# Performance work log

Measured on AMD Instinct MI355X. Metric: run time of the kernel, lower is better.

The kernel has to match this reference:

```python
import jax, jax.numpy as jnp
import numpy as np

BITS = 4
DIM = 64
N_LEVELS = 2 ** BITS


def _build_lloyd_max_codebook(bits=BITS, dim=DIM, n_samples=200000, n_iter=200, seed=0):
    """Lloyd-Max scalar quantizer for one coordinate of a random unit vector in R^dim."""
    rng = np.random.default_rng(seed)
    raw = rng.standard_normal((n_samples, dim)).astype(np.float32)
    unit = raw / np.linalg.norm(raw, axis=-1, keepdims=True)
    samples = unit[:, 0].astype(np.float64)
    n_levels = 2 ** bits
    sorted_samples = np.sort(samples)
    q_pos = np.linspace(0.5 / n_levels, 1.0 - 0.5 / n_levels, n_levels)
    idx_init = np.clip((q_pos * n_samples).astype(np.int64), 0, n_samples - 1)
    codebook = sorted_samples[idx_init].copy()
    for _ in range(n_iter):
        assignments = np.argmin(np.abs(samples[:, None] - codebook[None, :]), axis=1)
        counts = np.bincount(assignments, minlength=n_levels)
        sums = np.bincount(assignments, weights=samples, minlength=n_levels)
        new_cb = np.where(counts > 0, sums / np.maximum(counts, 1), codebook)
        delta = np.max(np.abs(new_cb - codebook))
        codebook = new_cb
        if delta < 1e-9:
            break
    return np.sort(codebook).astype(np.float32)


def _rotation_matrix(dim=DIM, seed=42):
    rng = np.random.default_rng(seed)
    g = rng.standard_normal((dim, dim)).astype(np.float32)
    q, _ = np.linalg.qr(g)
    return q.astype(np.float32)


def setup_inputs() -> dict:
    key = jax.random.key(0)
    x = jax.random.normal(key, (2, 32, 4096, DIM), dtype=jnp.float32)  # [B, H, S, dim]
    codebook = jnp.asarray(_build_lloyd_max_codebook())  # [16]
    R = jnp.asarray(_rotation_matrix())                  # [dim, dim]
    return {"x": x, "codebook": codebook, "R": R}


def reference(x, codebook, R):
    """TurboQuant round-trip: compress (norm -> rotate -> scalar quantize) then decompress."""
    x = x.astype(jnp.float32)
    # --- quantize ---
    scale = jnp.clip(jnp.linalg.norm(x, axis=-1, keepdims=True), 1e-8)  # [..., 1]
    z = (x / scale) @ R.T                                                # [..., dim]
    indices = jnp.argmin(jnp.abs(z[..., None] - codebook), axis=-1)      # [..., dim] int
    # --- dequantize ---
    z_hat = codebook[indices]        # [..., dim]
    x_rec = (z_hat @ R) * scale      # un-rotate, re-scale
    return x_rec
```

## Files before the change

kernel.cpp:

```cpp
#include <hip/hip_runtime.h>


#define TQ_D 64
#define TQ_NLEV 16

__global__ __launch_bounds__(256, 2) void tq_f32(
    const float* __restrict__ x,
    const float* __restrict__ cbk,
    const float* __restrict__ R,
    float* __restrict__ out,
    int nrows)
{
#pragma clang fp contract(off)
    int row = blockIdx.x * blockDim.x + threadIdx.x;
    if (row >= nrows) return;

    const float* xr = x + (size_t)row * TQ_D;

    float xs[TQ_D];
#pragma unroll
    for (int k = 0; k < TQ_D; k += 4) {
        float4 v = *reinterpret_cast<const float4*>(xr + k);
        xs[k] = v.x; xs[k + 1] = v.y; xs[k + 2] = v.z; xs[k + 3] = v.w;
    }

    float r8[8];
#pragma unroll
    for (int j = 0; j < 8; ++j) r8[j] = xs[j] * xs[j];
#pragma unroll
    for (int i = 8; i < TQ_D; i += 8) {
#pragma unroll
        for (int j = 0; j < 8; ++j) {
            float t = xs[i + j] * xs[i + j];
            r8[j] = r8[j] + t;
        }
    }
    float ss = ((r8[0] + r8[1]) + (r8[2] + r8[3])) + ((r8[4] + r8[5]) + (r8[6] + r8[7]));

    float scale = (float)sqrt((double)ss);
    scale = fmaxf(scale, 1e-8f);

#pragma unroll
    for (int k = 0; k < TQ_D; ++k)
        xs[k] = xs[k] / scale;

    float cb[TQ_NLEV];
#pragma unroll
    for (int i = 0; i < TQ_NLEV; ++i) cb[i] = cbk[i];

    float acc[TQ_D];
#pragma unroll
    for (int k = 0; k < TQ_D; ++k) acc[k] = 0.0f;

#pragma unroll 2
    for (int j = 0; j < TQ_D; ++j) {
        const float* rj = R + j * TQ_D;

        float z = 0.0f;
#pragma unroll
        for (int k = 0; k < TQ_D; ++k)
            z = fmaf(xs[k], rj[k], z);

        float best = fabsf(z - cb[0]);
        float zh = cb[0];
#pragma unroll
        for (int i = 1; i < TQ_NLEV; ++i) {
            float d = fabsf(z - cb[i]);
            bool c = d < best;
            best = c ? d : best;
            zh = c ? cb[i] : zh;
        }

#pragma unroll
        for (int k = 0; k < TQ_D; ++k)
            acc[k] = fmaf(zh, rj[k], acc[k]);
    }

    float* orow = out + (size_t)row * TQ_D;
#pragma unroll
    for (int k = 0; k < TQ_D; k += 4) {
        float4 v;
        v.x = acc[k]     * scale;
        v.y = acc[k + 1] * scale;
        v.z = acc[k + 2] * scale;
        v.w = acc[k + 3] * scale;
        *reinterpret_cast<float4*>(orow + k) = v;
    }
}

extern "C" void kernel_launch(void* const* d_in, const int* in_sizes, int n_in,
                              void* d_out, int out_size, void* d_ws, size_t ws_size,
                              hipStream_t stream) {
    const float* x   = (const float*)d_in[0];
    const float* cbk = (const float*)d_in[1];
    const float* R   = (const float*)d_in[2];
    float* out = (float*)d_out;

    const int nrows = in_sizes[0] / TQ_D;
    const int blocks = (nrows + 255) / 256;

    tq_f32<<<blocks, 256, 0, stream>>>(x, cbk, R, out, nrows);
}
```

Baseline: 301.3 us.

## Split fused quantize/reconstruct into two kernels via workspace

```diff
diff --git a/kernel.cpp b/kernel.cpp
--- a/kernel.cpp
+++ b/kernel.cpp
@@ -4,7 +4,126 @@
 #define TQ_D 64
 #define TQ_NLEV 16
 
-__global__ __launch_bounds__(256, 2) void tq_f32(
+__global__ __launch_bounds__(256) void tq_quant(
+    const float* __restrict__ x,
+    const float* __restrict__ cbk,
+    const float* __restrict__ R,
+    float* __restrict__ zh_ws,
+    float* __restrict__ scale_ws,
+    int nrows)
+{
+#pragma clang fp contract(off)
+    int row = blockIdx.x * blockDim.x + threadIdx.x;
+    if (row >= nrows) return;
+
+    const float* xr = x + (size_t)row * TQ_D;
+
+    float xs[TQ_D];
+#pragma unroll
+    for (int k = 0; k < TQ_D; k += 4) {
+        float4 v = *reinterpret_cast<const float4*>(xr + k);
+        xs[k] = v.x; xs[k + 1] = v.y; xs[k + 2] = v.z; xs[k + 3] = v.w;
+    }
+
+    float r8[8];
+#pragma unroll
+    for (int j = 0; j < 8; ++j) r8[j] = xs[j] * xs[j];
+#pragma unroll
+    for (int i = 8; i < TQ_D; i += 8) {
+#pragma unroll
+        for (int j = 0; j < 8; ++j) {
+            float t = xs[i + j] * xs[i + j];
+            r8[j] = r8[j] + t;
+        }
+    }
+    float ss = ((r8[0] + r8[1]) + (r8[2] + r8[3])) + ((r8[4] + r8[5]) + (r8[6] + r8[7]));
+
+    float scale = (float)sqrt((double)ss);
+    scale = fmaxf(scale, 1e-8f);
+
+#pragma unroll
+    for (int k = 0; k < TQ_D; ++k)
+        xs[k] = xs[k] / scale;
+
+    float cb[TQ_NLEV];
+#pragma unroll
+    for (int i = 0; i < TQ_NLEV; ++i) cb[i] = cbk[i];
+
+    float* zrow = zh_ws + (size_t)row * TQ_D;
+    for (int jq = 0; jq < TQ_D / 4; ++jq) {
+        float4 w;
+#pragma unroll
+        for (int t = 0; t < 4; ++t) {
+            const float* rj = R + (jq * 4 + t) * TQ_D;
+
+            float z = 0.0f;
+#pragma unroll
+            for (int k = 0; k < TQ_D; ++k)
+                z = fmaf(xs[k], rj[k], z);
+
+            float best = fabsf(z - cb[0]);
+            float zh = cb[0];
+#pragma unroll
+            for (int i = 1; i < TQ_NLEV; ++i) {
+                float d = fabsf(z - cb[i]);
+                bool c = d < best;
+                best = c ? d : best;
+                zh = c ? cb[i] : zh;
+            }
+            if      (t == 0) w.x = zh;
+            else if (t == 1) w.y = zh;
+            else if (t == 2) w.z = zh;
+            else             w.w = zh;
+        }
+        *reinterpret_cast<float4*>(zrow + jq * 4) = w;
+    }
+    scale_ws[row] = scale;
+}
+
+__global__ __launch_bounds__(256) void tq_recon(
+    const float* __restrict__ zh_ws,
+    const float* __restrict__ scale_ws,
+    const float* __restrict__ R,
+    float* __restrict__ out,
+    int nrows)
+{
+#pragma clang fp contract(off)
+    int row = blockIdx.x * blockDim.x + threadIdx.x;
+    if (row >= nrows) return;
+
+    const float* zrow = zh_ws + (size_t)row * TQ_D;
+    float scale = scale_ws[row];
+
+    float acc[TQ_D];
+#pragma unroll
+    for (int k = 0; k < TQ_D; ++k) acc[k] = 0.0f;
+
+#pragma unroll 2
+    for (int jq = 0; jq < TQ_D / 4; ++jq) {
+        float4 zq = *reinterpret_cast<const float4*>(zrow + jq * 4);
+#pragma unroll
+        for (int t = 0; t < 4; ++t) {
+            float zh = (t == 0) ? zq.x : (t == 1) ? zq.y : (t == 2) ? zq.z : zq.w;
+            const float* rj = R + (jq * 4 + t) * TQ_D;
+#pragma unroll
+            for (int k = 0; k < TQ_D; ++k)
+                acc[k] = fmaf(zh, rj[k], acc[k]);
+        }
+    }
+
+    float* orow = out + (size_t)row * TQ_D;
+#pragma unroll
+    for (int k = 0; k < TQ_D; k += 4) {
+        float4 v;
+        v.x = acc[k]     * scale;
+        v.y = acc[k + 1] * scale;
+        v.z = acc[k + 2] * scale;
+        v.w = acc[k + 3] * scale;
+        *reinterpret_cast<float4*>(orow + k) = v;
+    }
+}
+
+__global__ __launch_bounds__(256) void tq_fused(
     const float* __restrict__ x,
     const float* __restrict__ cbk,
     const float* __restrict__ R,
@@ -23,7 +142,6 @@
         float4 v = *reinterpret_cast<const float4*>(xr + k);
         xs[k] = v.x; xs[k + 1] = v.y; xs[k + 2] = v.z; xs[k + 3] = v.w;
     }
-
     float r8[8];
 #pragma unroll
     for (int j = 0; j < 8; ++j) r8[j] = xs[j] * xs[j];
@@ -36,13 +154,10 @@
         }
     }
     float ss = ((r8[0] + r8[1]) + (r8[2] + r8[3])) + ((r8[4] + r8[5]) + (r8[6] + r8[7]));
-
     float scale = (float)sqrt((double)ss);
     scale = fmaxf(scale, 1e-8f);
-
-#pragma unroll
-    for (int k = 0; k < TQ_D; ++k)
-        xs[k] = xs[k] / scale;
+#pragma unroll
+    for (int k = 0; k < TQ_D; ++k) xs[k] = xs[k] / scale;
 
     float cb[TQ_NLEV];
 #pragma unroll
@@ -55,12 +170,9 @@
 #pragma unroll 2
     for (int j = 0; j < TQ_D; ++j) {
         const float* rj = R + j * TQ_D;
-
         float z = 0.0f;
 #pragma unroll
-        for (int k = 0; k < TQ_D; ++k)
-            z = fmaf(xs[k], rj[k], z);
-
+        for (int k = 0; k < TQ_D; ++k) z = fmaf(xs[k], rj[k], z);
         float best = fabsf(z - cb[0]);
         float zh = cb[0];
 #pragma unroll
@@ -70,10 +182,8 @@
             best = c ? d : best;
             zh = c ? cb[i] : zh;
         }
-
-#pragma unroll
-        for (int k = 0; k < TQ_D; ++k)
-            acc[k] = fmaf(zh, rj[k], acc[k]);
+#pragma unroll
+        for (int k = 0; k < TQ_D; ++k) acc[k] = fmaf(zh, rj[k], acc[k]);
     }
 
     float* orow = out + (size_t)row * TQ_D;
@@ -99,5 +209,15 @@
     const int nrows = in_sizes[0] / TQ_D;
     const int blocks = (nrows + 255) / 256;
 
-    tq_f32<<<blocks, 256, 0, stream>>>(x, cbk, R, out, nrows);
-}
+    const size_t need = (size_t)nrows * TQ_D * sizeof(float)
+                      + (size_t)nrows * sizeof(float);
+
+    if (ws_size >= need) {
+        float* scale_ws = (float*)d_ws;
+        float* zh_ws    = scale_ws + nrows;
+        tq_quant<<<blocks, 256, 0, stream>>>(x, cbk, R, zh_ws, scale_ws, nrows);
+        tq_recon<<<blocks, 256, 0, stream>>>(zh_ws, scale_ws, R, out, nrows);
+    } else {
+        tq_fused<<<blocks, 256, 0, stream>>>(x, cbk, R, out, nrows);
+    }
+}
```

Result: faster. 276.1 us (-8.4%).
